# Performance work log

Hardware: AMD Instinct MI355X
Metric: run time of the kernel (lower is better)

The kernel has to match this reference:

```python
import jax, jax.numpy as jnp
import numpy as np

B, I, O, S, C = 64, 2048, 2048, 10, 512  # batch, input, output, dendritic segments, context dim


def setup_inputs() -> dict:
    key = jax.random.key(0)
    ks = jax.random.split(key, 8)
    x = jax.random.normal(ks[0], (B, I), dtype=jnp.float32)
    context = jax.random.normal(ks[1], (B, C), dtype=jnp.float32)
    prev_activation = jax.random.normal(ks[2], (B, I), dtype=jnp.float32)
    # sparse-initialized weight: randn/sqrt(I) * (rand > sparsity)
    w = jax.random.normal(ks[3], (O, I), dtype=jnp.float32) / np.sqrt(I)
    mask = (jax.random.uniform(ks[4], (O, I)) > 0.9).astype(jnp.float32)
    weight = w * mask
    bias = jnp.zeros((O,), dtype=jnp.float32)
    astrocyte_activation = jnp.ones((O,), dtype=jnp.float32)
    astrocyte_threshold = jnp.full((O,), 0.5, dtype=jnp.float32)
    dendrite_segments = jax.random.normal(ks[5], (O, I, S), dtype=jnp.float32) / np.sqrt(I)
    dendritic_gates = jnp.ones((O, S), dtype=jnp.float32)
    connection_strength = jnp.ones((O, I), dtype=jnp.float32)
    pruning_threshold = jnp.full((1,), 0.01, dtype=jnp.float32)
    return {
        "x": x, "context": context, "prev_activation": prev_activation,
        "weight": weight, "bias": bias,
        "astrocyte_activation": astrocyte_activation,
        "astrocyte_threshold": astrocyte_threshold,
        "dendrite_segments": dendrite_segments,
        "dendritic_gates": dendritic_gates,
        "connection_strength": connection_strength,
        "pruning_threshold": pruning_threshold,
    }


def reference(x, context, prev_activation, weight, bias, astrocyte_activation,
              astrocyte_threshold, dendrite_segments, dendritic_gates,
              connection_strength, pruning_threshold):
    dt = x.dtype
    # structural plasticity (eval branch): prune weak connections
    conn_mask = (jnp.abs(weight) * connection_strength > pruning_threshold[0]).astype(dt)
    eff_w = weight * conn_mask  # [O, I]
    # astrocyte modulation
    ctx_signal = jnp.mean(context, axis=-1, keepdims=True)          # [B, 1]
    astro = jax.nn.sigmoid(ctx_signal * astrocyte_activation[None, :])  # [B, O]
    astro = astro * (astro > astrocyte_threshold[None, :]).astype(dt)
    mean_astro = jnp.mean(astro, axis=0)                            # [O]
    mod_w = eff_w * mean_astro[:, None]                             # [O, I]
    synaptic = x @ mod_w.T + bias                                   # [B, O]
    # multi-compartment dendritic processing
    seg_act = jnp.einsum('bi,ois->bos', x, dendrite_segments)       # [B, O, S]
    gated = jax.nn.relu(seg_act) * jax.nn.sigmoid(dendritic_gates)[None, :, :]
    dendritic = jnp.sum(gated, axis=-1)                             # [B, O]
    return jax.nn.relu(synaptic + dendritic)
```

## Files before the change

kernel.cpp:

```cpp
#include <hip/hip_runtime.h>
#include <math.h>

#define Bn 64
#define In 2048
#define On 2048
#define Sn 10
#define Cn 512

#define KSPLIT 4
#define KRANGE (In / KSPLIT)
#define KT 64
#define NSTG (KRANGE / KT)
#define LROW 72
#define SROW 50
#define SLOT 12

typedef short short8 __attribute__((ext_vector_type(8)));
typedef float f32x4 __attribute__((ext_vector_type(4)));

__device__ __forceinline__ unsigned short f2bf(float f) {
    union { float f; unsigned u; } v; v.f = f;
    unsigned r = (v.u + 0x7FFFu + ((v.u >> 16) & 1u)) >> 16;
    return (unsigned short)r;
}

__global__ void prep_kernel(const float* __restrict__ x,
                            const float* __restrict__ ctx,
                            float* __restrict__ ws_ctx,
                            unsigned short* __restrict__ ws_xbf) {
    const int b = blockIdx.x;
    const int t = threadIdx.x;
    if (b < Bn) {
        __shared__ float red[256];
        red[t] = ctx[b * Cn + t] + ctx[b * Cn + t + 256];
        __syncthreads();
        for (int off = 128; off > 0; off >>= 1) {
            if (t < off) red[t] += red[t + off];
            __syncthreads();
        }
        if (t == 0) ws_ctx[b] = red[0] * (1.0f / (float)Cn);
    } else {
        int idx = (b - Bn) * 256 + t;
        ws_xbf[idx] = f2bf(x[idx]);
    }
}

__global__ void mastro_kernel(const float* __restrict__ aact,
                              const float* __restrict__ athr,
                              const float* __restrict__ ws_ctx,
                              float* __restrict__ ws_mastro) {
    const int o = blockIdx.x * 256 + threadIdx.x;
    const float aa = aact[o], th = athr[o];
    float sum = 0.0f;
    for (int b = 0; b < Bn; ++b) {
        float sg = 1.0f / (1.0f + expf(-ws_ctx[b] * aa));
        if (sg > th) sum += sg;
    }
    ws_mastro[o] = sum * (1.0f / (float)Bn);
}

__global__ __launch_bounds__(64, 2)
void main_kernel(const unsigned short* __restrict__ xbf,
                 const float* __restrict__ wgt,
                 const float* __restrict__ cst,
                 const float* __restrict__ seg,
                 const float* __restrict__ prn,
                 float* __restrict__ P) {
    __shared__ __align__(16) unsigned short Blds[2][48 * LROW];

    const int l = threadIdx.x;
    const int grp = blockIdx.x >> 2;
    const int ks  = blockIdx.x & 3;
    const int o0 = grp * 4;
    const int ib = ks * KRANGE;
    const int l15 = l & 15, q = l >> 4;
    const float pthr = prn[0];

    for (int idx = l; idx < 4 * LROW; idx += 64) {
        Blds[0][44 * LROW + idx] = 0;
        Blds[1][44 * LROW + idx] = 0;
    }

    const int ii0 = (2 * l) / 10;
    const int s0  = (2 * l) % 10;

    float2 sv[4][5];
    float wv[4], cv[4];

    auto load_stage = [&](int is) {
        const int k0 = ib + is * KT;
#pragma unroll
        for (int oo = 0; oo < 4; ++oo) {
            const float* sp = seg + ((size_t)(o0 + oo) * In + k0) * Sn + 2 * l;
#pragma unroll
            for (int c = 0; c < 5; ++c) sv[oo][c] = *(const float2*)(sp + c * 128);
            wv[oo] = wgt[(size_t)(o0 + oo) * In + k0 + l];
            cv[oo] = cst[(size_t)(o0 + oo) * In + k0 + l];
        }
    };

    auto store_stage = [&](int bb) {
#pragma unroll
        for (int oo = 0; oo < 4; ++oo) {
            int ii = ii0, s = s0;
#pragma unroll
            for (int c = 0; c < 5; ++c) {
                unsigned short* bp = &Blds[bb][(oo * 10 + s) * LROW + ii];
                bp[0]    = f2bf(sv[oo][c].x);
                bp[LROW] = f2bf(sv[oo][c].y);
                s += 8; ii += 12;
                if (s >= 10) { s -= 10; ++ii; }
            }
            float e = (__builtin_fabsf(wv[oo]) * cv[oo] > pthr) ? wv[oo] : 0.0f;
            Blds[bb][(40 + oo) * LROW + l] = f2bf(e);
        }
    };

    f32x4 acc[12];
#pragma unroll
    for (int n = 0; n < 12; ++n) acc[n] = (f32x4){0.f, 0.f, 0.f, 0.f};

    auto compute = [&](int bb, int is) {
        const int k0 = ib + is * KT;
#pragma unroll
        for (int kk = 0; kk < KT; kk += 32) {
            short8 a[4];
#pragma unroll
            for (int mt = 0; mt < 4; ++mt)
                a[mt] = *(const short8*)(xbf + (size_t)(mt * 16 + l15) * In + k0 + q * 8 + kk);
            short8 b0 = *(const short8*)&Blds[bb][(0  + l15) * LROW + q * 8 + kk];
            short8 b1 = *(const short8*)&Blds[bb][(16 + l15) * LROW + q * 8 + kk];
            short8 b2 = *(const short8*)&Blds[bb][(32 + l15) * LROW + q * 8 + kk];
#pragma unroll
            for (int mt = 0; mt < 4; ++mt) {
                acc[mt * 3 + 0] = __builtin_amdgcn_mfma_f32_16x16x32_bf16(a[mt], b0, acc[mt * 3 + 0], 0, 0, 0);
                acc[mt * 3 + 1] = __builtin_amdgcn_mfma_f32_16x16x32_bf16(a[mt], b1, acc[mt * 3 + 1], 0, 0, 0);
                acc[mt * 3 + 2] = __builtin_amdgcn_mfma_f32_16x16x32_bf16(a[mt], b2, acc[mt * 3 + 2], 0, 0, 0);
            }
        }
    };

    load_stage(0);
    store_stage(0);
    load_stage(1);
    for (int is = 0; is < NSTG; ++is) {
        compute(is & 1, is);
        if (is + 1 < NSTG) {
            store_stage((is + 1) & 1);
            if (is + 2 < NSTG) load_stage(is + 2);
        }
    }

    float* scratch = (float*)&Blds[0][0];
#pragma unroll
    for (int mt = 0; mt < 4; ++mt)
#pragma unroll
        for (int nt = 0; nt < 3; ++nt) {
            const int n = nt * 16 + l15;
            if (n < 44) {
#pragma unroll
                for (int r = 0; r < 4; ++r)
                    scratch[(mt * 16 + q * 4 + r) * SROW + n] = acc[mt * 3 + nt][r];
            }
        }
    const float* srow = scratch + l * SROW;
#pragma unroll
    for (int ol = 0; ol < 4; ++ol) {
        float d[10];
#pragma unroll
        for (int s = 0; s < 10; ++s) d[s] = srow[ol * 10 + s];
        const float syn = srow[40 + ol];
        f32x4 p0 = {d[0], d[1], d[2], d[3]};
        f32x4 p1 = {d[4], d[5], d[6], d[7]};
        f32x4 p2 = {d[8], d[9], syn, 0.0f};
        float* pp = P + (((size_t)ks * On + o0 + ol) * Bn + l) * SLOT;
        *(f32x4*)(pp)     = p0;
        *(f32x4*)(pp + 4) = p1;
        *(f32x4*)(pp + 8) = p2;
    }
}

__global__ void finalize_kernel(const float* __restrict__ P,
                                const float* __restrict__ gates,
                                const float* __restrict__ bias,
                                const float* __restrict__ ws_mastro,
                                float* __restrict__ out) {
    const int t = threadIdx.x;
    const int b = t & 63;
    const int ol = t >> 6;
    const int o = blockIdx.x * 4 + ol;
    f32x4 v0 = {0.f, 0.f, 0.f, 0.f}, v1 = v0, v2 = v0;
#pragma unroll
    for (int ks = 0; ks < KSPLIT; ++ks) {
        const f32x4* p = (const f32x4*)(P + (((size_t)ks * On + o) * Bn + b) * SLOT);
        v0 += p[0]; v1 += p[1]; v2 += p[2];
    }
    float d[12];
#pragma unroll
    for (int j = 0; j < 4; ++j) { d[j] = v0[j]; d[4 + j] = v1[j]; d[8 + j] = v2[j]; }
    float dend = 0.0f;
#pragma unroll
    for (int s = 0; s < Sn; ++s) {
        float g = 1.0f / (1.0f + expf(-gates[o * Sn + s]));
        float r = d[s] > 0.0f ? d[s] : 0.0f;
        dend += r * g;
    }
    float val = d[10] * ws_mastro[o] + bias[o] + dend;
    out[(size_t)b * On + o] = val > 0.0f ? val : 0.0f;
}

extern "C" void kernel_launch(void* const* d_in, const int* in_sizes, int n_in,
                              void* d_out, int out_size, void* d_ws, size_t ws_size,
                              hipStream_t stream) {
    (void)in_sizes; (void)n_in; (void)out_size; (void)ws_size;
    const float* x    = (const float*)d_in[0];
    const float* ctx  = (const float*)d_in[1];
    const float* wgt  = (const float*)d_in[3];
    const float* bias = (const float*)d_in[4];
    const float* aact = (const float*)d_in[5];
    const float* athr = (const float*)d_in[6];
    const float* seg  = (const float*)d_in[7];
    const float* gat  = (const float*)d_in[8];
    const float* cst  = (const float*)d_in[9];
    const float* prn  = (const float*)d_in[10];
    float* out = (float*)d_out;

    float* ws_ctx = (float*)d_ws;
    unsigned short* ws_xbf = (unsigned short*)((char*)d_ws + 256);
    float* ws_mastro = (float*)((char*)d_ws + 262400);
    float* ws_P = (float*)((char*)d_ws + 270592);

    prep_kernel<<<Bn + (Bn * In) / 256, 256, 0, stream>>>(x, ctx, ws_ctx, ws_xbf);
    mastro_kernel<<<On / 256, 256, 0, stream>>>(aact, athr, ws_ctx, ws_mastro);
    main_kernel<<<(On / 4) * KSPLIT, 64, 0, stream>>>(ws_xbf, wgt, cst, seg, prn, ws_P);
    finalize_kernel<<<On / 4, 256, 0, stream>>>(ws_P, gat, bias, ws_mastro, out);
}
```

Before: 300.1 us.

## Assign one output neuron per block, drop split-K, fuse epilogue and astrocyte reduction

```diff
diff --git a/kernel.cpp b/kernel.cpp
--- a/kernel.cpp
+++ b/kernel.cpp
@@ -7,13 +7,9 @@
 #define Sn 10
 #define Cn 512
 
-#define KSPLIT 4
-#define KRANGE (In / KSPLIT)
 #define KT 64
-#define NSTG (KRANGE / KT)
+#define NSTG (In / KT)
 #define LROW 72
-#define SROW 50
-#define SLOT 12
 
 typedef short short8 __attribute__((ext_vector_type(8)));
 typedef float f32x4 __attribute__((ext_vector_type(4)));
@@ -45,168 +41,149 @@
     }
 }
 
-__global__ void mastro_kernel(const float* __restrict__ aact,
-                              const float* __restrict__ athr,
-                              const float* __restrict__ ws_ctx,
-                              float* __restrict__ ws_mastro) {
-    const int o = blockIdx.x * 256 + threadIdx.x;
-    const float aa = aact[o], th = athr[o];
-    float sum = 0.0f;
-    for (int b = 0; b < Bn; ++b) {
-        float sg = 1.0f / (1.0f + expf(-ws_ctx[b] * aa));
-        if (sg > th) sum += sg;
-    }
-    ws_mastro[o] = sum * (1.0f / (float)Bn);
-}
-
 __global__ __launch_bounds__(64, 2)
 void main_kernel(const unsigned short* __restrict__ xbf,
                  const float* __restrict__ wgt,
                  const float* __restrict__ cst,
                  const float* __restrict__ seg,
                  const float* __restrict__ prn,
-                 float* __restrict__ P) {
-    __shared__ __align__(16) unsigned short Blds[2][48 * LROW];
+                 const float* __restrict__ gates,
+                 const float* __restrict__ bias,
+                 const float* __restrict__ aact,
+                 const float* __restrict__ athr,
+                 const float* __restrict__ ws_ctx,
+                 float* __restrict__ outT) {
+    __shared__ __align__(16) unsigned short Blds[2][16 * LROW];
 
     const int l = threadIdx.x;
-    const int grp = blockIdx.x >> 2;
-    const int ks  = blockIdx.x & 3;
-    const int o0 = grp * 4;
-    const int ib = ks * KRANGE;
+    const int o = blockIdx.x;
     const int l15 = l & 15, q = l >> 4;
     const float pthr = prn[0];
 
-    for (int idx = l; idx < 4 * LROW; idx += 64) {
-        Blds[0][44 * LROW + idx] = 0;
-        Blds[1][44 * LROW + idx] = 0;
+    for (int idx = l; idx < 5 * LROW; idx += 64) {
+        Blds[0][11 * LROW + idx] = 0;
+        Blds[1][11 * LROW + idx] = 0;
     }
 
     const int ii0 = (2 * l) / 10;
     const int s0  = (2 * l) % 10;
 
-    float2 sv[4][5];
-    float wv[4], cv[4];
-
-    auto load_stage = [&](int is) {
-        const int k0 = ib + is * KT;
-#pragma unroll
-        for (int oo = 0; oo < 4; ++oo) {
-            const float* sp = seg + ((size_t)(o0 + oo) * In + k0) * Sn + 2 * l;
-#pragma unroll
-            for (int c = 0; c < 5; ++c) sv[oo][c] = *(const float2*)(sp + c * 128);
-            wv[oo] = wgt[(size_t)(o0 + oo) * In + k0 + l];
-            cv[oo] = cst[(size_t)(o0 + oo) * In + k0 + l];
-        }
+    float2 sv[3][5];
+    float  wv[3], cv[3];
+    short8 av[3][8];
+
+    const float* segO = seg + (size_t)o * In * Sn;
+    const float* wgtO = wgt + (size_t)o * In;
+    const float* cstO = cst + (size_t)o * In;
+
+    auto load_stage = [&](int is, int sl) {
+        const int k0 = is * KT;
+        const float* sp = segO + (size_t)k0 * Sn + 2 * l;
+#pragma unroll
+        for (int c = 0; c < 5; ++c) sv[sl][c] = *(const float2*)(sp + c * 128);
+        wv[sl] = wgtO[k0 + l];
+        cv[sl] = cstO[k0 + l];
+#pragma unroll
+        for (int mt = 0; mt < 4; ++mt)
+#pragma unroll
+            for (int kk2 = 0; kk2 < 2; ++kk2)
+                av[sl][mt * 2 + kk2] =
+                    *(const short8*)(xbf + (size_t)(mt * 16 + l15) * In + k0 + kk2 * 32 + q * 8);
     };
 
-    auto store_stage = [&](int bb) {
-#pragma unroll
-        for (int oo = 0; oo < 4; ++oo) {
-            int ii = ii0, s = s0;
-#pragma unroll
-            for (int c = 0; c < 5; ++c) {
-                unsigned short* bp = &Blds[bb][(oo * 10 + s) * LROW + ii];
-                bp[0]    = f2bf(sv[oo][c].x);
-                bp[LROW] = f2bf(sv[oo][c].y);
-                s += 8; ii += 12;
-                if (s >= 10) { s -= 10; ++ii; }
-            }
-            float e = (__builtin_fabsf(wv[oo]) * cv[oo] > pthr) ? wv[oo] : 0.0f;
-            Blds[bb][(40 + oo) * LROW + l] = f2bf(e);
-        }
+    auto store_stage = [&](int sl, int bb) {
+        int ii = ii0, s = s0;
+#pragma unroll
+        for (int c = 0; c < 5; ++c) {
+            unsigned short* bp = &Blds[bb][s * LROW + ii];
+            bp[0]    = f2bf(sv[sl][c].x);
+            bp[LROW] = f2bf(sv[sl][c].y);
+            s += 8; ii += 12;
+            if (s >= 10) { s -= 10; ++ii; }
+        }
+        float e = (__builtin_fabsf(wv[sl]) * cv[sl] > pthr) ? wv[sl] : 0.0f;
+        Blds[bb][10 * LROW + l] = f2bf(e);
     };
 
-    f32x4 acc[12];
-#pragma unroll
-    for (int n = 0; n < 12; ++n) acc[n] = (f32x4){0.f, 0.f, 0.f, 0.f};
-
-    auto compute = [&](int bb, int is) {
-        const int k0 = ib + is * KT;
-#pragma unroll
-        for (int kk = 0; kk < KT; kk += 32) {
-            short8 a[4];
+    f32x4 acc[4];
+#pragma unroll
+    for (int n = 0; n < 4; ++n) acc[n] = (f32x4){0.f, 0.f, 0.f, 0.f};
+
+    auto compute = [&](int sl, int bb) {
+#pragma unroll
+        for (int kk2 = 0; kk2 < 2; ++kk2) {
+            short8 b8 = *(const short8*)&Blds[bb][l15 * LROW + kk2 * 32 + q * 8];
 #pragma unroll
             for (int mt = 0; mt < 4; ++mt)
-                a[mt] = *(const short8*)(xbf + (size_t)(mt * 16 + l15) * In + k0 + q * 8 + kk);
-            short8 b0 = *(const short8*)&Blds[bb][(0  + l15) * LROW + q * 8 + kk];
-            short8 b1 = *(const short8*)&Blds[bb][(16 + l15) * LROW + q * 8 + kk];
-            short8 b2 = *(const short8*)&Blds[bb][(32 + l15) * LROW + q * 8 + kk];
-#pragma unroll
-            for (int mt = 0; mt < 4; ++mt) {
-                acc[mt * 3 + 0] = __builtin_amdgcn_mfma_f32_16x16x32_bf16(a[mt], b0, acc[mt * 3 + 0], 0, 0, 0);
-                acc[mt * 3 + 1] = __builtin_amdgcn_mfma_f32_16x16x32_bf16(a[mt], b1, acc[mt * 3 + 1], 0, 0, 0);
-                acc[mt * 3 + 2] = __builtin_amdgcn_mfma_f32_16x16x32_bf16(a[mt], b2, acc[mt * 3 + 2], 0, 0, 0);
-            }
+                acc[mt] = __builtin_amdgcn_mfma_f32_16x16x32_bf16(av[sl][mt * 2 + kk2], b8,
+                                                                  acc[mt], 0, 0, 0);
         }
     };
 
-    load_stage(0);
-    store_stage(0);
-    load_stage(1);
+    load_stage(0, 0);
+    load_stage(1, 1);
+    store_stage(0, 0);
+    load_stage(2, 2);
     for (int is = 0; is < NSTG; ++is) {
-        compute(is & 1, is);
-        if (is + 1 < NSTG) {
-            store_stage((is + 1) & 1);
-            if (is + 2 < NSTG) load_stage(is + 2);
-        }
-    }
-
-    float* scratch = (float*)&Blds[0][0];
-#pragma unroll
-    for (int mt = 0; mt < 4; ++mt)
-#pragma unroll
-        for (int nt = 0; nt < 3; ++nt) {
-            const int n = nt * 16 + l15;
-            if (n < 44) {
-#pragma unroll
-                for (int r = 0; r < 4; ++r)
-                    scratch[(mt * 16 + q * 4 + r) * SROW + n] = acc[mt * 3 + nt][r];
-            }
-        }
-    const float* srow = scratch + l * SROW;
-#pragma unroll
-    for (int ol = 0; ol < 4; ++ol) {
-        float d[10];
-#pragma unroll
-        for (int s = 0; s < 10; ++s) d[s] = srow[ol * 10 + s];
-        const float syn = srow[40 + ol];
-        f32x4 p0 = {d[0], d[1], d[2], d[3]};
-        f32x4 p1 = {d[4], d[5], d[6], d[7]};
-        f32x4 p2 = {d[8], d[9], syn, 0.0f};
-        float* pp = P + (((size_t)ks * On + o0 + ol) * Bn + l) * SLOT;
-        *(f32x4*)(pp)     = p0;
-        *(f32x4*)(pp + 4) = p1;
-        *(f32x4*)(pp + 8) = p2;
-    }
-}
-
-__global__ void finalize_kernel(const float* __restrict__ P,
-                                const float* __restrict__ gates,
-                                const float* __restrict__ bias,
-                                const float* __restrict__ ws_mastro,
-                                float* __restrict__ out) {
-    const int t = threadIdx.x;
-    const int b = t & 63;
-    const int ol = t >> 6;
-    const int o = blockIdx.x * 4 + ol;
-    f32x4 v0 = {0.f, 0.f, 0.f, 0.f}, v1 = v0, v2 = v0;
-#pragma unroll
-    for (int ks = 0; ks < KSPLIT; ++ks) {
-        const f32x4* p = (const f32x4*)(P + (((size_t)ks * On + o) * Bn + b) * SLOT);
-        v0 += p[0]; v1 += p[1]; v2 += p[2];
-    }
-    float d[12];
-#pragma unroll
-    for (int j = 0; j < 4; ++j) { d[j] = v0[j]; d[4 + j] = v1[j]; d[8 + j] = v2[j]; }
+        const int sl = is % 3;
+        compute(sl, is & 1);
+        if (is + 1 < NSTG) store_stage((is + 1) % 3, (is + 1) & 1);
+        if (is + 3 < NSTG) load_stage(is + 3, sl);
+    }
+
+    float* sc = (float*)&Blds[0][0];
+    if (l15 < 12) {
+#pragma unroll
+        for (int mt = 0; mt < 4; ++mt)
+#pragma unroll
+            for (int r = 0; r < 4; ++r)
+                sc[(mt * 16 + q * 4 + r) * 12 + l15] = acc[mt][r];
+    }
+    float d[11];
+#pragma unroll
+    for (int j = 0; j < 11; ++j) d[j] = sc[l * 12 + j];
+
     float dend = 0.0f;
+    const float* gp = gates + o * Sn;
 #pragma unroll
     for (int s = 0; s < Sn; ++s) {
-        float g = 1.0f / (1.0f + expf(-gates[o * Sn + s]));
+        float g = 1.0f / (1.0f + expf(-gp[s]));
         float r = d[s] > 0.0f ? d[s] : 0.0f;
         dend += r * g;
     }
-    float val = d[10] * ws_mastro[o] + bias[o] + dend;
-    out[(size_t)b * On + o] = val > 0.0f ? val : 0.0f;
+    float sg = 1.0f / (1.0f + expf(-ws_ctx[l] * aact[o]));
+    float contrib = (sg > athr[o]) ? sg : 0.0f;
+#pragma unroll
+    for (int off = 32; off > 0; off >>= 1) contrib += __shfl_xor(contrib, off);
+    const float mastro = contrib * (1.0f / 64.0f);
+
+    float val = d[10] * mastro + bias[o] + dend;
+    outT[(size_t)o * Bn + l] = val > 0.0f ? val : 0.0f;
+}
+
+__global__ void transpose_kernel(const float* __restrict__ outT,
+                                 float* __restrict__ out) {
+    __shared__ float tile[64][65];
+    const int t = threadIdx.x;
+    const int o0 = blockIdx.x * 64;
+    {
+        const int b = t & 63;
+        const int o4 = t >> 6;
+#pragma unroll
+        for (int r = 0; r < 16; ++r) {
+            const int oi = o4 * 16 + r;
+            tile[oi][b] = outT[(size_t)(o0 + oi) * Bn + b];
+        }
+    }
+    __syncthreads();
+    {
+        const int oi = t & 63;
+#pragma unroll
+        for (int r = 0; r < 16; ++r) {
+            const int b = (t >> 6) * 16 + r;
+            out[(size_t)b * On + o0 + oi] = tile[oi][b];
+        }
+    }
 }
 
 extern "C" void kernel_launch(void* const* d_in, const int* in_sizes, int n_in,
@@ -227,11 +204,10 @@
 
     float* ws_ctx = (float*)d_ws;
     unsigned short* ws_xbf = (unsigned short*)((char*)d_ws + 256);
-    float* ws_mastro = (float*)((char*)d_ws + 262400);
-    float* ws_P = (float*)((char*)d_ws + 270592);
+    float* ws_outT = (float*)((char*)d_ws + 262400);
 
     prep_kernel<<<Bn + (Bn * In) / 256, 256, 0, stream>>>(x, ctx, ws_ctx, ws_xbf);
-    mastro_kernel<<<On / 256, 256, 0, stream>>>(aact, athr, ws_ctx, ws_mastro);
-    main_kernel<<<(On / 4) * KSPLIT, 64, 0, stream>>>(ws_xbf, wgt, cst, seg, prn, ws_P);
-    finalize_kernel<<<On / 4, 256, 0, stream>>>(ws_P, gat, bias, ws_mastro, out);
-}
+    main_kernel<<<On, 64, 0, stream>>>(ws_xbf, wgt, cst, seg, prn, gat, bias,
+                                       aact, athr, ws_ctx, ws_outT);
+    transpose_kernel<<<On / 64, 256, 0, stream>>>(ws_outT, out);
+}
```

New measurement: 572.3 us. 1.91x slower.
